# Kernel tuning notes

Measured on AMD Instinct MI355X. Metric: run time of the kernel, lower is better.

Reference implementation:

```python
import jax, jax.numpy as jnp
import numpy as np

TEMPERATURE = 1.0  # module's set_temperature value; mode=False path: out = x + attn_out * temperature


def setup_inputs() -> dict:
    key = jax.random.key(0)
    ks = jax.random.split(key, 7)
    B, C, H, W = 4, 256, 64, 64
    Cqk = C // 8
    s = 0.02
    return {
        "x": jax.random.normal(ks[0], (B, C, H, W), dtype=jnp.float32),
        "Wq": jax.random.normal(ks[1], (Cqk, C), dtype=jnp.float32) * s,
        "bq": jax.random.normal(ks[2], (Cqk,), dtype=jnp.float32) * s,
        "Wk": jax.random.normal(ks[3], (Cqk, C), dtype=jnp.float32) * s,
        "bk": jax.random.normal(ks[4], (Cqk,), dtype=jnp.float32) * s,
        "Wv": jax.random.normal(ks[5], (C, C), dtype=jnp.float32) * s,
        "bv": jax.random.normal(ks[6], (C,), dtype=jnp.float32) * s,
    }


def reference(x, Wq, bq, Wk, bk, Wv, bv):
    B, C, H, W = x.shape
    N = H * W
    xf = x.reshape(B, C, N)                      # flatten spatial -> tokens
    # 1x1 convs == pointwise linear over channels
    q = jnp.einsum('oc,bcn->bno', Wq, xf) + bq            # [B, N, Cqk]
    k = jnp.einsum('oc,bcn->bon', Wk, xf) + bk[:, None]   # [B, Cqk, N]
    attn = jax.nn.softmax(jnp.einsum('bno,bom->bnm', q, k), axis=-1)  # [B, N, N]
    v = jnp.einsum('oc,bcn->bon', Wv, xf) + bv[:, None]   # [B, C, N]
    # torch: bmm(value, attn^T) -> out[b,c,m] = sum_n v[b,c,n] * attn[b,m,n]
    out = jnp.einsum('bcn,bmn->bcm', v, attn).reshape(B, C, H, W)
    return x + out * TEMPERATURE
```

## Files before the change

### kernel.cpp

```cpp
#include <hip/hip_runtime.h>

#define BATCH 4
#define CH    256
#define NTOK  4096
#define DQK   32

typedef __attribute__((ext_vector_type(4))) float  f32x4;
typedef __attribute__((ext_vector_type(2))) float  f32x2;
typedef __attribute__((ext_vector_type(8))) __bf16 bf16x8;
typedef __attribute__((ext_vector_type(2))) unsigned int u32x2;
typedef __attribute__((ext_vector_type(4))) unsigned int u32x4;

static __device__ __forceinline__ unsigned short f2bf(float f) {
    unsigned int u = __builtin_bit_cast(unsigned int, f);
    unsigned int r = u + 0x7FFFu + ((u >> 16) & 1u);
    return (unsigned short)(r >> 16);
}
static __device__ __forceinline__ unsigned int pack2(float a, float b) {
    return (unsigned int)f2bf(a) | ((unsigned int)f2bf(b) << 16);
}
static __device__ __forceinline__ unsigned int cvt_pk_bf16(float a, float b) {
    unsigned int r;
    asm("v_cvt_pk_bf16_f32 %0, %1, %2" : "=v"(r) : "v"(a), "v"(b));
    return r;
}

__global__ __launch_bounds__(256)
void wconv(const float* __restrict__ Wq, const float* __restrict__ Wk,
           const float* __restrict__ Wv, unsigned short* __restrict__ Wbf,
           unsigned int* __restrict__ Mk)
{
    if (blockIdx.x == 0 && threadIdx.x < BATCH) Mk[threadIdx.x] = 0u;
    const int id = (blockIdx.x * 256 + threadIdx.x) * 4;
    const int r  = id >> 8;
    const int c  = id & 255;
    const float* src = (r < 32) ? (Wq + r * 256 + c)
                     : (r < 64) ? (Wk + (r - 32) * 256 + c)
                                : (Wv + (size_t)(r - 64) * 256 + c);
    float v0 = src[0], v1 = src[1], v2 = src[2], v3 = src[3];
    u32x2 p = {pack2(v0, v1), pack2(v2, v3)};
    *reinterpret_cast<u32x2*>(Wbf + id) = p;
}

__global__ __launch_bounds__(256, 4)
void qkv_proj(const float* __restrict__ x,
              const float* __restrict__ pbq, const float* __restrict__ pbk,
              const float* __restrict__ pbv,
              const unsigned short* __restrict__ Wbf,
              unsigned short* __restrict__ Qh,
              unsigned short* __restrict__ Kh,
              unsigned short* __restrict__ Vh,
              unsigned int* __restrict__ Mk)
{
    const int t    = threadIdx.x;
    const int wave = t >> 6;
    const int lane = t & 63;
    const int low  = lane & 15;
    const int quad = lane >> 4;
    const int tok0 = blockIdx.x * 16;
    const int b    = tok0 >> 12;
    const int nl0  = tok0 & (NTOK - 1);

    __shared__ unsigned short ob[256 * 24];

    f32x4 acc[5];
    #pragma unroll
    for (int j = 0; j < 5; ++j) {
        const int rtg = wave * 5 + j;
        float bb = (rtg < 2) ? pbq[rtg * 16 + low]
                 : (rtg < 4) ? pbk[(rtg - 2) * 16 + low]
                             : pbv[(rtg - 4) * 16 + low];
        f32x4 z = {bb, bb, bb, bb};
        acc[j] = z;
    }

    const float* xb = x + (size_t)b * CH * NTOK + nl0 + low;

    #pragma unroll
    for (int k0 = 0; k0 < 8; ++k0) {
        const int cbase = k0 * 32 + quad * 8;
        float xv[8];
        #pragma unroll
        for (int e = 0; e < 8; ++e)
            xv[e] = xb[(size_t)(cbase + e) * NTOK];
        u32x4 ap = {cvt_pk_bf16(xv[0], xv[1]), cvt_pk_bf16(xv[2], xv[3]),
                    cvt_pk_bf16(xv[4], xv[5]), cvt_pk_bf16(xv[6], xv[7])};
        const bf16x8 af = __builtin_bit_cast(bf16x8, ap);
        #pragma unroll
        for (int j = 0; j < 5; ++j) {
            const int rtg = wave * 5 + j;
            const bf16x8 bf = *reinterpret_cast<const bf16x8*>(
                Wbf + (size_t)(rtg * 16 + low) * 256 + k0 * 32 + quad * 8);
            acc[j] = __builtin_amdgcn_mfma_f32_16x16x32_bf16(af, bf, acc[j], 0, 0, 0);
        }
    }

    #pragma unroll
    for (int j = 0; j < 5; ++j) {
        const int rtg = wave * 5 + j;
        if (rtg < 4) {
            unsigned short* dst = (rtg < 2) ? Qh : Kh;
            const int wr = (rtg & 1) * 16 + low;
            #pragma unroll
            for (int reg = 0; reg < 4; ++reg) {
                const int token = tok0 + quad * 4 + reg;
                dst[(size_t)token * DQK + wr] = f2bf(acc[j][reg]);
            }
        }
    }
    if (wave == 0) {
        f32x4 kk = acc[2] * acc[2] + acc[3] * acc[3];
        #pragma unroll
        for (int mask = 1; mask <= 8; mask <<= 1)
            #pragma unroll
            for (int reg = 0; reg < 4; ++reg)
                kk[reg] += __shfl_xor(kk[reg], mask);
        if (low == 0) {
            #pragma unroll
            for (int reg = 0; reg < 4; ++reg)
                atomicMax(&Mk[b], __builtin_bit_cast(unsigned int, kk[reg]));
        }
    }

    #pragma unroll
    for (int j = 0; j < 5; ++j) {
        const int rtg = wave * 5 + j;
        if (rtg >= 4) {
            const int c = (rtg - 4) * 16 + low;
            #pragma unroll
            for (int reg = 0; reg < 4; ++reg)
                ob[c * 24 + quad * 4 + reg] = f2bf(acc[j][reg]);
        }
    }
    __syncthreads();
    {
        const unsigned int* obd = (const unsigned int*)ob;
        const int h = t & 1;
        #pragma unroll
        for (int pass = 0; pass < 2; ++pass) {
            const int c = (t >> 1) + pass * 128;
            const u32x4 v = *reinterpret_cast<const u32x4*>(obd + c * 12 + h * 4);
            *reinterpret_cast<u32x4*>(
                Vh + ((size_t)b * CH + c) * NTOK + nl0 + h * 8) = v;
        }
    }
}

__global__ __launch_bounds__(512, 2)
void attn(const float* __restrict__ x,
          const unsigned short* __restrict__ Qh,
          const unsigned short* __restrict__ Kh,
          const unsigned short* __restrict__ Vh,
          const unsigned int* __restrict__ Mk,
          float* __restrict__ out)
{
    const int t    = threadIdx.x;
    const int wave = t >> 6;
    const int kg   = wave & 3;
    const int ch   = wave >> 2;
    const int lane = t & 63;
    const int low  = lane & 15;
    const int quad = lane >> 4;

    const int beta = blockIdx.x;
    const int b    = (beta & 7) >> 1;
    const int q0   = (((beta >> 3) * 2) + (beta & 1)) * 64;

    __shared__ float smem[36864 + 256];
    unsigned int* Pbase = (unsigned int*)smem;
    float* lbuf = smem + 36864;

    const float LOG2E = 1.44269504088896f;

    bf16x8 qfrag[4];
    float  m2[4];
    {
        const float M2 = __builtin_bit_cast(float, Mk[b]);
        #pragma unroll
        for (int j = 0; j < 4; ++j) {
            qfrag[j] = *reinterpret_cast<const bf16x8*>(
                Qh + (size_t)(b * NTOK + q0 + j * 16 + low) * DQK + quad * 8);
            float qn2 = 0.f;
            #pragma unroll
            for (int e = 0; e < 8; ++e) {
                float qv = (float)qfrag[j][e];
                qn2 += qv * qv;
            }
            qn2 += __shfl_xor(qn2, 16);
            qn2 += __shfl_xor(qn2, 32);
            m2[j] = __builtin_sqrtf(qn2 * M2) * (1.02f * LOG2E);
        }
    }

    f32x4 acc[4][8];
    #pragma unroll
    for (int qs = 0; qs < 4; ++qs)
        #pragma unroll
        for (int ct = 0; ct < 8; ++ct) { f32x4 z = {0.f,0.f,0.f,0.f}; acc[qs][ct] = z; }
    float l_s[4] = {0.f, 0.f, 0.f, 0.f};

    const unsigned short* Kb = Kh + (size_t)b * NTOK * DQK;
    const unsigned short* Vb = Vh + (size_t)b * CH * NTOK;

    #define S_PHASE(ii, buf)                                                    \
    {                                                                           \
        const int n0s = ((ii) * 4 + kg) * 64;                                   \
        bf16x8 kf[4];                                                           \
        _Pragma("unroll")                                                       \
        for (int kt = 0; kt < 4; ++kt)                                          \
            kf[kt] = *reinterpret_cast<const bf16x8*>(                          \
                Kb + (size_t)(n0s + kt * 16 + low) * DQK + quad * 8);           \
        _Pragma("unroll")                                                       \
        for (int j = 0; j < 4; ++j) {                                           \
            f32x4 S[4];                                                         \
            _Pragma("unroll")                                                   \
            for (int kt = 0; kt < 4; ++kt) {                                    \
                f32x4 z = {0.f,0.f,0.f,0.f};                                    \
                S[kt] = __builtin_amdgcn_mfma_f32_16x16x32_bf16(kf[kt],         \
                            qfrag[j], z, 0, 0, 0);                              \
            }                                                                   \
            float sum = 0.f;                                                    \
            unsigned int* pq = Pbase + (buf) * 18432 + wave * 2304              \
                               + (j * 16 + low) * 36 + quad * 2;                \
            _Pragma("unroll")                                                   \
            for (int kt = 0; kt < 4; ++kt) {                                    \
                float p0 = __builtin_amdgcn_exp2f(S[kt][0] * LOG2E - m2[j]);    \
                float p1 = __builtin_amdgcn_exp2f(S[kt][1] * LOG2E - m2[j]);    \
                float p2 = __builtin_amdgcn_exp2f(S[kt][2] * LOG2E - m2[j]);    \
                float p3 = __builtin_amdgcn_exp2f(S[kt][3] * LOG2E - m2[j]);    \
                sum += (p0 + p1) + (p2 + p3);                                   \
                u32x2 w2 = {cvt_pk_bf16(p0, p1), cvt_pk_bf16(p2, p3)};          \
                *reinterpret_cast<u32x2*>(pq + kt * 8) = w2;                    \
            }                                                                   \
            l_s[j] += sum;                                                      \
        }                                                                       \
    }

    S_PHASE(0, 0)

    for (int i = 0; i < 16; ++i) {
        if (i < 15) S_PHASE(i + 1, (i + 1) & 1)

        {
            const int n0 = (i * 4 + kg) * 64;
            const unsigned short* Phh =
                (const unsigned short*)(Pbase + (i & 1) * 18432 + wave * 2304);
            __builtin_amdgcn_s_setprio(1);
            #pragma unroll
            for (int s = 0; s < 2; ++s) {
                bf16x8 pf[4];
                #pragma unroll
                for (int qs = 0; qs < 4; ++qs)
                    pf[qs] = *reinterpret_cast<const bf16x8*>(
                        Phh + (qs * 16 + low) * 72 + s * 32 + quad * 8);
                #pragma unroll
                for (int ct = 0; ct < 8; ++ct) {
                    const bf16x8 vf = *reinterpret_cast<const bf16x8*>(
                        Vb + (size_t)(ch * 128 + ct * 16 + low) * NTOK
                           + n0 + s * 32 + quad * 8);
                    #pragma unroll
                    for (int qs = 0; qs < 4; ++qs)
                        acc[qs][ct] = __builtin_amdgcn_mfma_f32_16x16x32_bf16(
                            vf, pf[qs], acc[qs][ct], 0, 0, 0);
                }
            }
            __builtin_amdgcn_s_setprio(0);
        }
    }
    #undef S_PHASE

    #pragma unroll
    for (int j = 0; j < 4; ++j) {
        l_s[j] += __shfl_xor(l_s[j], 16);
        l_s[j] += __shfl_xor(l_s[j], 32);
    }
    if (quad == 0) {
        #pragma unroll
        for (int jj = 0; jj < 2; ++jj) {
            const int qs = 2 * ch + jj;
            lbuf[kg * 64 + qs * 16 + low] = l_s[qs];
        }
    }
    __syncthreads();

    const int q = t & 63;
    const int u = t >> 6;
    float invl = 0.f;
    for (int rd = 0; rd < 8; ++rd) {
        #pragma unroll
        for (int qs = 0; qs < 4; ++qs) {
            float* sl = smem + wave * 1408 + (qs * 16 + low) * 22 + quad * 4;
            f32x2 lo = {acc[qs][rd][0], acc[qs][rd][1]};
            f32x2 hi = {acc[qs][rd][2], acc[qs][rd][3]};
            *reinterpret_cast<f32x2*>(sl)     = lo;
            *reinterpret_cast<f32x2*>(sl + 2) = hi;
        }
        __syncthreads();
        if (rd == 0)
            invl = 1.0f / (((lbuf[q] + lbuf[64 + q]) + (lbuf[128 + q] + lbuf[192 + q])));

        #pragma unroll
        for (int p = 0; p < 4; ++p) {
            const int half = p >> 1;
            const int c15  = u * 2 + (p & 1);
            const int wb   = half * 4;
            float O = (smem[(wb + 0) * 1408 + q * 22 + c15]
                     + smem[(wb + 1) * 1408 + q * 22 + c15])
                    + (smem[(wb + 2) * 1408 + q * 22 + c15]
                     + smem[(wb + 3) * 1408 + q * 22 + c15]);
            const int c = half * 128 + rd * 16 + c15;
            const size_t idx = (size_t)(b * CH + c) * NTOK + q0 + q;
            out[idx] = x[idx] + O * invl;
        }
        __syncthreads();
    }
}

extern "C" void kernel_launch(void* const* d_in, const int* in_sizes, int n_in,
                              void* d_out, int out_size, void* d_ws, size_t ws_size,
                              hipStream_t stream) {
    const float* x  = (const float*)d_in[0];
    const float* Wq = (const float*)d_in[1];
    const float* bq = (const float*)d_in[2];
    const float* Wk = (const float*)d_in[3];
    const float* bk = (const float*)d_in[4];
    const float* Wv = (const float*)d_in[5];
    const float* bv = (const float*)d_in[6];
    float* out = (float*)d_out;

    unsigned short* Qh  = (unsigned short*)d_ws;
    unsigned short* Kh  = Qh  + (size_t)BATCH * NTOK * DQK;
    unsigned short* Vh  = Kh  + (size_t)BATCH * NTOK * DQK;
    unsigned short* Wbf = Vh  + (size_t)BATCH * CH * NTOK;
    unsigned int*   Mk  = (unsigned int*)(Wbf + 320 * 256);

    wconv<<<dim3(80), dim3(256), 0, stream>>>(Wq, Wk, Wv, Wbf, Mk);
    qkv_proj<<<dim3(1024), dim3(256), 0, stream>>>(x, bq, bk, bv, Wbf,
                                                   Qh, Kh, Vh, Mk);
    attn<<<dim3(256), dim3(512), 0, stream>>>(x, Qh, Kh, Vh, Mk, out);
}
```

Baseline: 222.5 us.

## Stage x tile in LDS and compute 32 tokens per block in qkv_proj

The projection kernel now handles 32 tokens per block instead of 16. It first loads the x tile with coalesced vector reads into LDS as bf16, then builds MFMA A-fragments from LDS. Each weight fragment loaded from global memory is reused for two token sub-tiles, which halves weight traffic per token and replaces strided scalar global loads of x. The cost is more LDS, more accumulator registers (launch bounds lowered to 2), and half as many blocks. The qkv projection is a small part of the total runtime, which is dominated by the attention kernel.

```diff
diff --git a/kernel.cpp b/kernel.cpp
--- a/kernel.cpp
+++ b/kernel.cpp
@@ -42,7 +42,7 @@
     *reinterpret_cast<u32x2*>(Wbf + id) = p;
 }
 
-__global__ __launch_bounds__(256, 4)
+__global__ __launch_bounds__(256, 2)
 void qkv_proj(const float* __restrict__ x,
               const float* __restrict__ pbq, const float* __restrict__ pbk,
               const float* __restrict__ pbv,
@@ -57,13 +57,28 @@
     const int lane = t & 63;
     const int low  = lane & 15;
     const int quad = lane >> 4;
-    const int tok0 = blockIdx.x * 16;
-    const int b    = tok0 >> 12;
-    const int nl0  = tok0 & (NTOK - 1);
-
-    __shared__ unsigned short ob[256 * 24];
-
-    f32x4 acc[5];
+    const int blk  = blockIdx.x;
+    const int b    = blk >> 7;
+    const int tok0 = (blk & 127) * 32;
+
+    __shared__ unsigned short xs[256 * 38];
+
+    {
+        const float* xg = x + (size_t)b * CH * NTOK + tok0;
+        const int k  = t & 7;
+        const int c0 = t >> 3;
+        #pragma unroll
+        for (int p = 0; p < 8; ++p) {
+            const int c = p * 32 + c0;
+            const f32x4 v = *reinterpret_cast<const f32x4*>(
+                xg + (size_t)c * NTOK + k * 4);
+            unsigned int* dst = reinterpret_cast<unsigned int*>(xs + c * 38 + k * 4);
+            dst[0] = cvt_pk_bf16(v[0], v[1]);
+            dst[1] = cvt_pk_bf16(v[2], v[3]);
+        }
+    }
+
+    f32x4 acc[5][2];
     #pragma unroll
     for (int j = 0; j < 5; ++j) {
         const int rtg = wave * 5 + j;
@@ -71,27 +86,33 @@
                  : (rtg < 4) ? pbk[(rtg - 2) * 16 + low]
                              : pbv[(rtg - 4) * 16 + low];
         f32x4 z = {bb, bb, bb, bb};
-        acc[j] = z;
-    }
-
-    const float* xb = x + (size_t)b * CH * NTOK + nl0 + low;
+        acc[j][0] = z; acc[j][1] = z;
+    }
+
+    __syncthreads();
 
     #pragma unroll
     for (int k0 = 0; k0 < 8; ++k0) {
-        const int cbase = k0 * 32 + quad * 8;
-        float xv[8];
-        #pragma unroll
-        for (int e = 0; e < 8; ++e)
-            xv[e] = xb[(size_t)(cbase + e) * NTOK];
-        u32x4 ap = {cvt_pk_bf16(xv[0], xv[1]), cvt_pk_bf16(xv[2], xv[3]),
-                    cvt_pk_bf16(xv[4], xv[5]), cvt_pk_bf16(xv[6], xv[7])};
-        const bf16x8 af = __builtin_bit_cast(bf16x8, ap);
+        bf16x8 wf[5];
         #pragma unroll
         for (int j = 0; j < 5; ++j) {
             const int rtg = wave * 5 + j;
-            const bf16x8 bf = *reinterpret_cast<const bf16x8*>(
+            wf[j] = *reinterpret_cast<const bf16x8*>(
                 Wbf + (size_t)(rtg * 16 + low) * 256 + k0 * 32 + quad * 8);
-            acc[j] = __builtin_amdgcn_mfma_f32_16x16x32_bf16(af, bf, acc[j], 0, 0, 0);
+        }
+        #pragma unroll
+        for (int tt = 0; tt < 2; ++tt) {
+            const unsigned short* xsrc = xs + (k0 * 32 + quad * 8) * 38 + tt * 16 + low;
+            unsigned int w0 = (unsigned int)xsrc[0 * 38] | ((unsigned int)xsrc[1 * 38] << 16);
+            unsigned int w1 = (unsigned int)xsrc[2 * 38] | ((unsigned int)xsrc[3 * 38] << 16);
+            unsigned int w2 = (unsigned int)xsrc[4 * 38] | ((unsigned int)xsrc[5 * 38] << 16);
+            unsigned int w3 = (unsigned int)xsrc[6 * 38] | ((unsigned int)xsrc[7 * 38] << 16);
+            u32x4 ap = {w0, w1, w2, w3};
+            const bf16x8 af = __builtin_bit_cast(bf16x8, ap);
+            #pragma unroll
+            for (int j = 0; j < 5; ++j)
+                acc[j][tt] = __builtin_amdgcn_mfma_f32_16x16x32_bf16(
+                    af, wf[j], acc[j][tt], 0, 0, 0);
         }
     }
 
@@ -102,46 +123,54 @@
             unsigned short* dst = (rtg < 2) ? Qh : Kh;
             const int wr = (rtg & 1) * 16 + low;
             #pragma unroll
-            for (int reg = 0; reg < 4; ++reg) {
-                const int token = tok0 + quad * 4 + reg;
-                dst[(size_t)token * DQK + wr] = f2bf(acc[j][reg]);
+            for (int tt = 0; tt < 2; ++tt)
+                #pragma unroll
+                for (int reg = 0; reg < 4; ++reg) {
+                    const int token = tok0 + tt * 16 + quad * 4 + reg;
+                    dst[(size_t)(b * NTOK + token) * DQK + wr] = f2bf(acc[j][tt][reg]);
+                }
+        }
+    }
+    if (wave == 0) {
+        #pragma unroll
+        for (int tt = 0; tt < 2; ++tt) {
+            f32x4 kk = acc[2][tt] * acc[2][tt] + acc[3][tt] * acc[3][tt];
+            #pragma unroll
+            for (int mask = 1; mask <= 8; mask <<= 1)
+                #pragma unroll
+                for (int reg = 0; reg < 4; ++reg)
+                    kk[reg] += __shfl_xor(kk[reg], mask);
+            if (low == 0) {
+                #pragma unroll
+                for (int reg = 0; reg < 4; ++reg)
+                    atomicMax(&Mk[b], __builtin_bit_cast(unsigned int, kk[reg]));
             }
         }
     }
-    if (wave == 0) {
-        f32x4 kk = acc[2] * acc[2] + acc[3] * acc[3];
-        #pragma unroll
-        for (int mask = 1; mask <= 8; mask <<= 1)
-            #pragma unroll
-            for (int reg = 0; reg < 4; ++reg)
-                kk[reg] += __shfl_xor(kk[reg], mask);
-        if (low == 0) {
-            #pragma unroll
-            for (int reg = 0; reg < 4; ++reg)
-                atomicMax(&Mk[b], __builtin_bit_cast(unsigned int, kk[reg]));
-        }
-    }
-
+
+    __syncthreads();
     #pragma unroll
     for (int j = 0; j < 5; ++j) {
         const int rtg = wave * 5 + j;
         if (rtg >= 4) {
             const int c = (rtg - 4) * 16 + low;
             #pragma unroll
-            for (int reg = 0; reg < 4; ++reg)
-                ob[c * 24 + quad * 4 + reg] = f2bf(acc[j][reg]);
+            for (int tt = 0; tt < 2; ++tt)
+                #pragma unroll
+                for (int reg = 0; reg < 4; ++reg)
+                    xs[c * 36 + tt * 16 + quad * 4 + reg] = f2bf(acc[j][tt][reg]);
         }
     }
     __syncthreads();
     {
-        const unsigned int* obd = (const unsigned int*)ob;
-        const int h = t & 1;
-        #pragma unroll
-        for (int pass = 0; pass < 2; ++pass) {
-            const int c = (t >> 1) + pass * 128;
-            const u32x4 v = *reinterpret_cast<const u32x4*>(obd + c * 12 + h * 4);
-            *reinterpret_cast<u32x4*>(
-                Vh + ((size_t)b * CH + c) * NTOK + nl0 + h * 8) = v;
+        const int k  = t & 7;
+        const int c0 = t >> 3;
+        #pragma unroll
+        for (int p = 0; p < 8; ++p) {
+            const int c = p * 32 + c0;
+            const u32x2 v = *reinterpret_cast<const u32x2*>(xs + c * 36 + k * 4);
+            *reinterpret_cast<u32x2*>(
+                Vh + ((size_t)b * CH + c) * NTOK + tok0 + k * 4) = v;
         }
     }
 }
@@ -335,7 +364,7 @@
     unsigned int*   Mk  = (unsigned int*)(Wbf + 320 * 256);
 
     wconv<<<dim3(80), dim3(256), 0, stream>>>(Wq, Wk, Wv, Wbf, Mk);
-    qkv_proj<<<dim3(1024), dim3(256), 0, stream>>>(x, bq, bk, bv, Wbf,
-                                                   Qh, Kh, Vh, Mk);
+    qkv_proj<<<dim3(512), dim3(256), 0, stream>>>(x, bq, bk, bv, Wbf,
+                                                  Qh, Kh, Vh, Mk);
     attn<<<dim3(256), dim3(512), 0, stream>>>(x, Qh, Kh, Vh, Mk, out);
 }
```

Result: faster. 214.1 us, median of 2 (-3.8%).
